# Performance work log

Measured on AMD Instinct MI355X. Metric: run time of the kernel, lower is better.

The kernel has to match this reference:

```python
import jax, jax.numpy as jnp
import numpy as np

V = 50000      # tokenizer vocab size
E = 128        # embedding_dim
H = 160        # encoder_hidden_dim (bidirectional -> 2H)
D = 196        # decoder_hidden_dim
A = 224        # attention_dim
BN = 56        # bottle_neck_dim
PAD, START, END, UNK = 0, 1, 2, 3
COV_FACTOR = 0.75


def _lstm_step(x, h, c, Wi, Wh, bi, bh):
    # torch gate order: i, f, g, o
    g = x @ Wi.T + h @ Wh.T + bi + bh
    i, f, gg, o = jnp.split(g, 4, axis=-1)
    c = jax.nn.sigmoid(f) * c + jax.nn.sigmoid(i) * jnp.tanh(gg)
    h = jax.nn.sigmoid(o) * jnp.tanh(c)
    return h, c


def _run_lstm(x_tbe, Wi, Wh, bi, bh):
    B = x_tbe.shape[1]
    Hh = Wh.shape[1]
    def step(carry, xt):
        h, c = carry
        h, c = _lstm_step(xt, h, c, Wi, Wh, bi, bh)
        return (h, c), h
    init = (jnp.zeros((B, Hh), x_tbe.dtype), jnp.zeros((B, Hh), x_tbe.dtype))
    (hT, cT), hs = jax.lax.scan(step, init, x_tbe)
    return hs, hT, cT


def setup_inputs() -> dict:
    key = jax.random.key(0)
    ks = iter(jax.random.split(key, 48))
    def rn(shape, s=0.05):
        return jax.random.normal(next(ks), shape, jnp.float32) * s
    B, Tin, Ttgt = 32, 256, 100
    inp = {
        'batch_input_ids': jax.random.randint(next(ks), (B, Tin), 0, V + 50, dtype=jnp.int32),
        'batch_target_ids': jax.random.randint(next(ks), (B, Ttgt), 0, V + 50, dtype=jnp.int32),
        'max_num_oovs': 50,
        'emb': rn((V, E), 0.1),
        # bidirectional encoder LSTM
        'Wi_f': rn((4 * H, E)), 'Wh_f': rn((4 * H, H)),
        'bi_f': jnp.zeros(4 * H), 'bh_f': jnp.zeros(4 * H),
        'Wi_b': rn((4 * H, E)), 'Wh_b': rn((4 * H, H)),
        'bi_b': jnp.zeros(4 * H), 'bh_b': jnp.zeros(4 * H),
        # enc->dec bridges
        'Weh': rn((D, 2 * H)), 'beh': jnp.zeros(D),
        'Wec': rn((D, 2 * H)), 'bec': jnp.zeros(D),
        # decoder LSTMCell
        'Wi_d': rn((4 * D, E)), 'Wh_d': rn((4 * D, D)),
        'bi_d': jnp.zeros(4 * D), 'bh_d': jnp.zeros(4 * D),
        # attention
        'Wea': rn((A, 2 * H)), 'bea': jnp.zeros(A),
        'Wda': rn((A, D)),
        'Wca': rn((A, 1)),
        'v_attn': rn((1, A)),
        # vocab projection (bottleneck)
        'W1': rn((BN, D + 2 * H)), 'b1': jnp.zeros(BN),
        'W2': rn((V - END, BN)), 'b2': jnp.zeros(V - END),
        # p_gen switch
        'Wcs': rn((1, 2 * H)), 'bcs': jnp.zeros(1),
        'Wds': rn((1, D)),
        'Wes': rn((1, E)),
    }
    return inp


def reference(batch_input_ids, batch_target_ids, max_num_oovs, emb,
              Wi_f, Wh_f, bi_f, bh_f, Wi_b, Wh_b, bi_b, bh_b,
              Weh, beh, Wec, bec, Wi_d, Wh_d, bi_d, bh_d,
              Wea, bea, Wda, Wca, v_attn, W1, b1, W2, b2,
              Wcs, bcs, Wds, Wes):
    B, Tin = batch_input_ids.shape
    # map OOV input ids to <unk> for embedding lookup
    in_mapped = jnp.where(batch_input_ids >= V, UNK, batch_input_ids)
    x_tbe = emb[in_mapped].transpose(1, 0, 2)          # [Tin,B,E]
    hs_f, hTf, cTf = _run_lstm(x_tbe, Wi_f, Wh_f, bi_f, bh_f)
    hs_b, hTb, cTb = _run_lstm(x_tbe[::-1], Wi_b, Wh_b, bi_b, bh_b)
    enc = jnp.concatenate([hs_f, hs_b[::-1]], -1).transpose(1, 0, 2)  # [B,Tin,2H]
    h = jnp.concatenate([hTf, hTb], -1) @ Weh.T + beh   # [B,D]
    c = jnp.concatenate([cTf, cTb], -1) @ Wec.T + bec   # [B,D]
    enc_attn = enc @ Wea.T + bea                        # [B,Tin,A] (loop-invariant)
    pad_mask = batch_input_ids == PAD
    wca = Wca[:, 0]                                     # [A]
    cov0 = jnp.zeros((B, Tin))
    cur0 = jnp.full((B,), START, jnp.int32)

    def step(carry, nt):
        h, c, cov, cur, nll, cl = carry
        e = emb[cur]                                     # [B,E]
        h, c = _lstm_step(e, h, c, Wi_d, Wh_d, bi_d, bh_d)
        s = jnp.tanh(enc_attn + (h @ Wda.T)[:, None, :] + cov[:, :, None] * wca)
        s = s @ v_attn[0]                                # [B,Tin]
        s = jnp.where(pad_mask, -jnp.inf, s)
        attn = jax.nn.softmax(s, axis=1)                 # [B,Tin]
        ctx = jnp.einsum('bt,bth->bh', attn, enc)        # [B,2H]
        hc = jnp.concatenate([h, ctx], -1)
        vocab = jax.nn.softmax(jnp.tanh(hc @ W1.T + b1) @ W2.T + b2, axis=1)  # [B,V-END]
        p_gen = jax.nn.sigmoid(ctx @ Wcs[0] + bcs[0] + h @ Wds[0] + e @ Wes[0])  # [B]
        # F.pad(vocab, (END, max_num_oovs)).gather(1, nt): left-pad END zeros,
        # right-pad OOV zeros -> gen prob is vocab[nt-END] if END<=nt<V else 0
        idx = jnp.clip(nt - END, 0, vocab.shape[1] - 1)
        gen_p = jnp.take_along_axis(vocab, idx[:, None], axis=1)[:, 0]
        gen_p = jnp.where((nt >= END) & (nt < V), gen_p, 0.0)
        copy_p = jnp.sum(attn * (batch_input_ids == nt[:, None]), axis=1)
        p = p_gen * gen_p + (1.0 - p_gen) * copy_p
        nll = nll - jnp.log(p + 1e-9)
        cl = cl + jnp.minimum(attn, cov).sum(axis=1)
        cov = cov + attn
        cur = jnp.where(nt >= V, UNK, nt)
        return (h, c, cov, cur, nll, cl), None

    (h, c, cov, cur, nll, cl), _ = jax.lax.scan(
        step, (h, c, cov0, cur0, jnp.zeros(B), jnp.zeros(B)), batch_target_ids.T)
    nll_loss = nll.sum()
    cov_loss = cl.sum()
    return nll_loss, cov_loss, nll_loss + COV_FACTOR * cov_loss
```

## Files before the change

### kernel.cpp

```cpp
#include <hip/hip_runtime.h>

#define MSCOPE __HIP_MEMORY_SCOPE_AGENT


constexpr size_t oXf   = 0;
constexpr size_t oXb   = oXf   + (size_t)8192*640;
constexpr size_t oXd   = oXb   + (size_t)8192*640;
constexpr size_t oHencB= oXd   + (size_t)3200*784;
constexpr size_t oEncA = oHencB+ (size_t)64*256*160;
constexpr size_t oEs   = oEncA + (size_t)8192*224;
constexpr size_t oCT   = oEs   + 3200;
constexpr size_t oH0   = oCT   + 10240;
constexpr size_t oC0   = oH0   + 6272;
constexpr size_t oHWdsAll = oC0 + 6272;
constexpr size_t oCtxWAll = oHWdsAll + 3200;
constexpr size_t oCopyAll = oCtxWAll + 3200;
constexpr size_t oZidxAll = oCopyAll + 3200;
constexpr size_t oClAll   = oZidxAll + 3200;
constexpr size_t oNllWg   = oClAll + 32;
constexpr size_t oW1cT    = oNllWg + 192;
constexpr size_t oFEnd    = oW1cT + 17920;
constexpr size_t oHdAll   = 0;
constexpr size_t oUAll    = oHdAll + (size_t)100*6272;
constexpr size_t oUPreAll = oUAll  + (size_t)100*1792;
constexpr size_t oHwdaAll = oUPreAll + (size_t)100*1792;
constexpr size_t oPartAll = oHwdaAll + (size_t)100*7168;
#define FENC(d,t,p)  ((((d)*256 + (t))*20 + (p))*16)
#define FLSTM(s,p)   (163840 + ((s)*25 + (p))*16)
#define FAUX(s,p)    (203840 + ((s)*8 + (p))*16)
#define FP2(s,m,p)   (216640 + (((s)*4 + (m))*32 + (p))*16)
#define CP3          421440
#define CFIN         421456
constexpr int fEnd = 421472;

__device__ __forceinline__ float fast_tanh(float x){
  float e = __expf(-2.f*fabsf(x));
  float r = (1.f - e) * __builtin_amdgcn_rcpf(1.f + e);
  return copysignf(r, x);
}
__device__ __forceinline__ float sigm(float x){
  return __builtin_amdgcn_rcpf(1.f + __expf(-x));
}
__device__ __forceinline__ float aload(const float* p){
  return __hip_atomic_load(const_cast<float*>(p), __ATOMIC_RELAXED, MSCOPE);
}
__device__ __forceinline__ float2 aload2(const float* p){
  unsigned long long u = __hip_atomic_load(
      reinterpret_cast<unsigned long long*>(const_cast<float*>(p)),
      __ATOMIC_RELAXED, MSCOPE);
  float2 r; __builtin_memcpy(&r, &u, 8); return r;
}
__device__ __forceinline__ void astore(float* p, float v){
  __hip_atomic_store(p, v, __ATOMIC_RELAXED, MSCOPE);
}
__device__ __forceinline__ void set_line(unsigned* line){
  __hip_atomic_store(line, 1u, __ATOMIC_RELAXED, MSCOPE);
}
template<int SLP>
__device__ __forceinline__ void wait_lines(unsigned* base, int n, int tid){
  if (tid < 64){
    for(;;){
      bool miss = (tid < n) &&
        (__hip_atomic_load(base + tid*16, __ATOMIC_RELAXED, MSCOPE) == 0u);
      if (__ballot(miss) == 0ULL) break;
      __builtin_amdgcn_s_sleep(SLP);
    }
  }
  __syncthreads();
}
__device__ __forceinline__ void add1(unsigned* word){
  (void)__hip_atomic_fetch_add(word, 1u, __ATOMIC_RELAXED, MSCOPE);
}
__device__ __forceinline__ float block_sum(float v, float* red){
  #pragma unroll
  for (int o=32;o;o>>=1) v += __shfl_down(v,o);
  if ((threadIdx.x&63)==0) red[threadIdx.x>>6] = v;
  __syncthreads();
  v = red[0]+red[1]+red[2]+red[3];
  __syncthreads();
  return v;
}

__global__ void prep_kernel(const int* __restrict__ in_ids, const int* __restrict__ tgt,
                            int* __restrict__ in_mapped, int* __restrict__ cur_ids,
                            unsigned* __restrict__ flags){
  const int g0 = blockIdx.x*256 + threadIdx.x, stride = gridDim.x*256;
  for (int i = g0; i < 8192; i += stride){
    int t = i >> 5, b = i & 31;
    int id = in_ids[b*256 + t];
    in_mapped[i] = (id >= 50000) ? 3 : id;
  }
  for (int i = g0; i < 3200; i += stride){
    int k = i >> 5, b = i & 31;
    int id = (k == 0) ? 1 : tgt[b*100 + (k-1)];
    cur_ids[i] = (id >= 50000) ? 3 : id;
  }
  for (int i = g0; i < fEnd; i += stride) flags[i] = 0u;
}

__global__ void w1c_transpose(const float* __restrict__ W1, float* __restrict__ W1cT){
  int i = blockIdx.x*256 + threadIdx.x;
  if (i < 17920){ int q = i / 56, g = i - q*56; W1cT[q*56+g] = W1[(size_t)g*516 + 196 + q]; }
}

struct RGArgs{ const int* gid; const float* emb; const float* W;
               const float* bias1; const float* bias2; float* out; int N; };
__global__ void __launch_bounds__(256) rowgemm(RGArgs a){
  __shared__ float rl[8*128];
  const int tid = threadIdx.x;
  const int N = a.N;
  const size_t r0 = (size_t)blockIdx.x*8;
  const size_t t = r0 >> 5; const int b0 = (int)(r0 & 31);
  for (int i = tid; i < 8*128; i += 256){
    int r = i >> 7, k = i & 127;
    rl[i] = a.emb[(size_t)a.gid[r0+r]*128 + k];
  }
  __syncthreads();
  for (int g = tid; g < N; g += 256){
    const float* wr = a.W + (size_t)g*128;
    float acc[8];
    #pragma unroll
    for (int r=0;r<8;r++) acc[r]=0.f;
    for (int k=0;k<128;k+=4){
      float4 wv = *(const float4*)(wr+k);
      #pragma unroll
      for (int r=0;r<8;r++){
        float4 xv = *(const float4*)(rl + r*128 + k);
        acc[r] += wv.x*xv.x + wv.y*xv.y + wv.z*xv.z + wv.w*xv.w;
      }
    }
    float bias = a.bias1[g] + a.bias2[g];
    float* op = a.out + ((size_t)t*N + g)*32 + b0;
    *(float4*)(op)   = make_float4(acc[0]+bias,acc[1]+bias,acc[2]+bias,acc[3]+bias);
    *(float4*)(op+4) = make_float4(acc[4]+bias,acc[5]+bias,acc[6]+bias,acc[7]+bias);
  }
}

__global__ void es_kernel(const int* __restrict__ gid, const float* __restrict__ emb,
                          const float* __restrict__ Wes, float* __restrict__ es){
  int r = blockIdx.x, l = threadIdx.x;
  const float* e = emb + (size_t)gid[r]*128;
  float acc = e[l]*Wes[l] + e[l+64]*Wes[l+64];
  #pragma unroll
  for (int o=32;o;o>>=1) acc += __shfl_down(acc,o);
  if (l==0) es[r] = acc;
}

struct EncArgs{ const float* Xf; const float* Xb; const float* Whf; const float* Whb;
                float* hencB; float* cT; unsigned* flg; };
__global__ void __launch_bounds__(256) enc_scan(EncArgs a){
  extern __shared__ float sm[];
  float* Wl = sm;
  float* hl = sm + 5120;
  const int wg = blockIdx.x;
  const int dir = wg/20, jwg = wg%20;
  const int tid = threadIdx.x;
  const int b = tid & 31, jl = tid >> 5;
  const int j = jwg*8 + jl;
  const float* Wh = dir ? a.Whb : a.Whf;
  const float* X  = dir ? a.Xb  : a.Xf;
  float* HB = a.hencB + (size_t)dir*32*256*160;
  unsigned* flg = a.flg;
  for (int i = tid; i < 32*160; i += 256){
    int row = i/160, k = i - row*160;
    int gate = row >> 3, jj = row & 7;
    Wl[i] = Wh[((size_t)(gate*160 + jwg*8 + jj))*160 + k];
  }
  for (int i = tid; i < 32*164; i += 256) hl[i] = 0.f;
  float c = 0.f;
  const float4* w0 = (const float4*)(Wl + (0*8+jl)*160);
  const float4* w1 = (const float4*)(Wl + (1*8+jl)*160);
  const float4* w2 = (const float4*)(Wl + (2*8+jl)*160);
  const float4* w3 = (const float4*)(Wl + (3*8+jl)*160);
  __syncthreads();
  for (int t = 0; t < 256; ++t){
    const int trow = dir ? 255 - t : t;
    const float* xr = X + ((size_t)trow*640 + j)*32 + b;
    float g0 = xr[0], g1 = xr[5120], g2 = xr[10240], g3 = xr[15360];
    if (t > 0){
      wait_lines<2>(flg + FENC(dir, t-1, 0), 20, tid);
      const int tprev = dir ? (256 - t) : (t-1);
      for (int i2 = tid; i2 < 2560; i2 += 256){
        int bb = i2/80, kk = (i2 - bb*80)*2;
        float2 v = aload2(HB + ((size_t)bb*256 + tprev)*160 + kk);
        *(float2*)(hl + bb*164 + kk) = v;
      }
    }
    __syncthreads();
    const float4* hr = (const float4*)(hl + b*164);
    #pragma unroll 4
    for (int q = 0; q < 40; ++q){
      float4 hv = hr[q];
      float4 a0 = w0[q], a1 = w1[q], a2 = w2[q], a3 = w3[q];
      g0 += hv.x*a0.x + hv.y*a0.y + hv.z*a0.z + hv.w*a0.w;
      g1 += hv.x*a1.x + hv.y*a1.y + hv.z*a1.z + hv.w*a1.w;
      g2 += hv.x*a2.x + hv.y*a2.y + hv.z*a2.z + hv.w*a2.w;
      g3 += hv.x*a3.x + hv.y*a3.y + hv.z*a3.z + hv.w*a3.w;
    }
    float ig = sigm(g0), fg = sigm(g1), gc = fast_tanh(g2), og = sigm(g3);
    c = fg*c + ig*gc;
    float h = og * fast_tanh(c);
    astore(&HB[((size_t)b*256 + trow)*160 + j], h);
    __syncthreads();
    if (tid == 0) set_line(flg + FENC(dir, t, jwg));
  }
  a.cT[dir*5120 + b*160 + j] = c;
}

__global__ void mid_kernel(const float* __restrict__ hencB, const float* __restrict__ cT,
                           const float* __restrict__ Weh, const float* __restrict__ beh,
                           const float* __restrict__ Wec, const float* __restrict__ bec,
                           float* __restrict__ h0, float* __restrict__ c0){
  __shared__ float hc[320], cc[320];
  int b = blockIdx.x, tid = threadIdx.x;
  if (tid < 160){
    hc[tid]     = hencB[((size_t)b*256 + 255)*160 + tid];
    hc[160+tid] = hencB[((size_t)(32+b)*256 + 0)*160 + tid];
    cc[tid]     = cT[b*160 + tid];
    cc[160+tid] = cT[5120 + b*160 + tid];
  }
  __syncthreads();
  for (int g = tid; g < 196; g += 256){
    const float* w1 = Weh + (size_t)g*320;
    const float* w2 = Wec + (size_t)g*320;
    float a1 = beh[g], a2 = bec[g];
    for (int k = 0; k < 320; ++k){ a1 += hc[k]*w1[k]; a2 += cc[k]*w2[k]; }
    h0[b*196 + g] = a1;
    c0[b*196 + g] = a2;
  }
}

__global__ void __launch_bounds__(256) encA_gemm(const float* __restrict__ hencB,
                 const float* __restrict__ Wea, const float* __restrict__ bea,
                 float* __restrict__ encA){
  __shared__ float rl[8*320];
  const int tid = threadIdx.x;
  const size_t r0 = (size_t)blockIdx.x*8;
  for (int i = tid; i < 8*320; i += 256){
    int r = i/320, k = i - r*320;
    size_t row = r0 + r; int b = (int)(row >> 8), t = (int)(row & 255);
    rl[i] = (k < 160) ? hencB[((size_t)b*256 + t)*160 + k]
                      : hencB[((size_t)(32+b)*256 + t)*160 + (k-160)];
  }
  __syncthreads();
  for (int g = tid; g < 224; g += 256){
    const float* wr = Wea + (size_t)g*320;
    float acc[8];
    #pragma unroll
    for (int r=0;r<8;r++) acc[r]=0.f;
    for (int k=0;k<320;k+=4){
      float4 wv = *(const float4*)(wr+k);
      #pragma unroll
      for (int r=0;r<8;r++){
        float4 xv = *(const float4*)(rl + r*320 + k);
        acc[r] += wv.x*xv.x + wv.y*xv.y + wv.z*xv.z + wv.w*xv.w;
      }
    }
    float bias = bea[g];
    #pragma unroll
    for (int r=0;r<8;r++) encA[(r0+r)*224 + g] = acc[r] + bias;
  }
}

struct DecArgs{
  const float* Xd; const float* hencB; const float* encA;
  const float* h0; const float* c0;
  const float* Whd; const float* Wda; const float* Wca; const float* vat;
  const float* W1; const float* b1; const float* W1cT; const float* W2; const float* b2;
  const float* Wcs; const float* bcs; const float* Wds; const float* es;
  const int* in_ids; const int* tgt;
  float* hdAll; float* uAll; float* uPreAll; float* hwdaAll;
  float* hWdsAll; float* ctxWAll; float* copyAll;
  float* zidxAll; float* partAll; float* clAll; float* nllWg; float* out;
  unsigned* flg;
};

__device__ __forceinline__ void load_scr(const float* hp, float* scr, int tid){
  for (int i2 = tid; i2 < 3136; i2 += 256){
    float2 hv = aload2(hp + i2*2);
    int e = i2*2; int b2 = e & 31; int j2 = e >> 5;
    scr[b2*204 + j2]     = hv.x;
    scr[(b2+1)*204 + j2] = hv.y;
  }
}

__global__ void __launch_bounds__(256) dec_scan(DecArgs A){
  extern __shared__ float sm[];
  const int wg = blockIdx.x, tid = threadIdx.x;
  const int bp = tid & 31, jl = tid >> 5;
  unsigned* flg = A.flg;

  if (wg < 25){
    const int wl = wg;
    const int j = wl*8 + jl;
    float* Wl  = sm;
    float* scr = sm + 6272;
    for (int i = tid; i < 32*196; i += 256){
      int row = i/196, k = i - row*196;
      int gate = row >> 3, jj = row & 7;
      int jg = wl*8 + jj;
      Wl[i] = (jg < 196) ? A.Whd[((size_t)(gate*196 + jg))*196 + k] : 0.f;
    }
    float c = (j < 196) ? A.c0[bp*196 + j] : 0.f;
    for (int i = tid; i < 6272; i += 256){
      int bb = i/196, k = i - bb*196;
      scr[bb*204 + k] = A.h0[i];
    }
    const float4* w0 = (const float4*)(Wl + (0*8+jl)*196);
    const float4* w1 = (const float4*)(Wl + (1*8+jl)*196);
    const float4* w2 = (const float4*)(Wl + (2*8+jl)*196);
    const float4* w3 = (const float4*)(Wl + (3*8+jl)*196);
    __syncthreads();
    for (int s = 0; s < 100; ++s){
      float x0=0.f,x1=0.f,x2=0.f,x3=0.f;
      if (j < 196){
        const float* xr = A.Xd + ((size_t)s*784 + j)*32 + bp;
        x0 = xr[0]; x1 = xr[6272]; x2 = xr[12544]; x3 = xr[18816];
      }
      if (s > 0){
        wait_lines<2>(flg + FLSTM(s-1, 0), 25, tid);
        load_scr(A.hdAll + (size_t)(s-1)*6272, scr, tid);
      }
      __syncthreads();
      if (j < 196){
        float g0=x0,g1=x1,g2=x2,g3=x3;
        const float4* hr = (const float4*)(scr + bp*204);
        #pragma unroll 7
        for (int q = 0; q < 49; ++q){
          float4 hv = hr[q];
          float4 a0 = w0[q], a1 = w1[q], a2 = w2[q], a3 = w3[q];
          g0 += hv.x*a0.x + hv.y*a0.y + hv.z*a0.z + hv.w*a0.w;
          g1 += hv.x*a1.x + hv.y*a1.y + hv.z*a1.z + hv.w*a1.w;
          g2 += hv.x*a2.x + hv.y*a2.y + hv.z*a2.z + hv.w*a2.w;
          g3 += hv.x*a3.x + hv.y*a3.y + hv.z*a3.z + hv.w*a3.w;
        }
        float ig = sigm(g0), fg = sigm(g1), gc = fast_tanh(g2), og = sigm(g3);
        c = fg*c + ig*gc;
        float h = og * fast_tanh(c);
        astore(&A.hdAll[(size_t)s*6272 + j*32 + bp], h);
      }
      __syncthreads();
      if (tid == 0) set_line(flg + FLSTM(s, wl));
    }
    return;
  }

  if (wg < 33){
    const int a_ = wg - 25;
    float* wdaL = sm;
    float* w1hL = sm + 5488;
    float* WdsL = sm + 6860;
    float* scr  = sm + 7056;
    for (int i = tid; i < 28*196; i += 256){
      int al = i/196, k = i - al*196;
      wdaL[i] = A.Wda[(size_t)(a_*28 + al)*196 + k];
    }
    for (int i = tid; i < 7*196; i += 256){
      int gl = i/196, k = i - gl*196;
      w1hL[i] = A.W1[(size_t)(a_*7 + gl)*516 + k];
    }
    if (a_ == 7) for (int i = tid; i < 196; i += 256) WdsL[i] = A.Wds[i];
    __syncthreads();
    for (int s = 0; s < 100; ++s){
      wait_lines<2>(flg + FLSTM(s, 0), 25, tid);
      load_scr(A.hdAll + (size_t)s*6272, scr, tid);
      __syncthreads();
      for (int i = tid; i < 896; i += 256){
        int b2 = i & 31, al = i >> 5;
        const float4* h4 = (const float4*)(scr + b2*204);
        const float4* w4 = (const float4*)(wdaL + al*196);
        float acc = 0.f;
        #pragma unroll 7
        for (int q = 0; q < 49; ++q){
          float4 a4 = h4[q], b4 = w4[q];
          acc += a4.x*b4.x + a4.y*b4.y + a4.z*b4.z + a4.w*b4.w;
        }
        astore(&A.hwdaAll[(size_t)s*7168 + b2*224 + a_*28 + al], acc);
      }
      if (tid < 224){
        int b2 = tid & 31, gl = tid >> 5;
        int g = a_*7 + gl;
        const float4* h4 = (const float4*)(scr + b2*204);
        const float4* w4 = (const float4*)(w1hL + gl*196);
        float acc = A.b1[g];
        #pragma unroll 7
        for (int q = 0; q < 49; ++q){
          float4 a4 = h4[q], b4 = w4[q];
          acc += a4.x*b4.x + a4.y*b4.y + a4.z*b4.z + a4.w*b4.w;
        }
        astore(&A.uPreAll[(size_t)s*1792 + b2*56 + g], acc);
      }
      if (a_ == 7 && tid < 32){
        const float* hb = scr + tid*204;
        float acc = 0.f;
        #pragma unroll 4
        for (int q = 0; q < 196; ++q) acc += hb[q]*WdsL[q];
        astore(&A.hWdsAll[s*32 + tid], acc);
      }
      __syncthreads();
      if (tid == 0) set_line(flg + FAUX(s, a_));
    }
    return;
  }

  if (wg < 65){
    const int b = wg - 33;
    float* hwdaL = sm;
    float* attnL = sm + 224;
    float* pctx  = sm + 480;
    float* ctxL  = sm + 1440;
    float* red   = sm + 1760;
    float* pu    = sm + 1764;
    float* wcaL  = sm + 1988;
    float* vL    = sm + 2212;
    float* WcsL  = sm + 2436;
    if (tid < 224){ wcaL[tid] = A.Wca[tid]; vL[tid] = A.vat[tid]; }
    for (int i = tid; i < 320; i += 256) WcsL[i] = A.Wcs[i];
    const int inid = A.in_ids[b*256 + tid];
    const float4* erow = (const float4*)(A.encA + (size_t)(b*256 + tid)*224);
    float cov = 0.f, clr = 0.f;
    __syncthreads();
    for (int s = 0; s < 100; ++s){
      wait_lines<2>(flg + FAUX(s, 0), 8, tid);
      if (tid < 224) hwdaL[tid] = aload(&A.hwdaAll[(size_t)s*7168 + b*224 + tid]);
      __syncthreads();
      float exv = 0.f;
      if (inid != 0){
        float acc = 0.f;
        #pragma unroll 8
        for (int q = 0; q < 56; ++q){
          float4 ev = erow[q]; int a0 = 4*q;
          acc += fast_tanh(ev.x + hwdaL[a0]   + cov*wcaL[a0]  )*vL[a0];
          acc += fast_tanh(ev.y + hwdaL[a0+1] + cov*wcaL[a0+1])*vL[a0+1];
          acc += fast_tanh(ev.z + hwdaL[a0+2] + cov*wcaL[a0+2])*vL[a0+2];
          acc += fast_tanh(ev.w + hwdaL[a0+3] + cov*wcaL[a0+3])*vL[a0+3];
        }
        exv = __expf(acc);
      }
      float S = block_sum(exv, red);
      float attn = exv * __builtin_amdgcn_rcpf(S);
      attnL[tid] = attn;
      const int ntb = A.tgt[b*100 + s];
      float cpS = block_sum((inid == ntb) ? attn : 0.f, red);
      float mnS = block_sum(fminf(attn, cov), red);
      if (tid == 0){
        astore(&A.copyAll[s*32 + b], cpS);
        clr += mnS;
        if (s == 99) astore(&A.clAll[b], clr);
      }
      cov += attn;
      if (tid < 240){
        int seg = tid/80, h4i = tid - seg*80;
        int t0 = seg*86, t1 = (t0+86 < 256) ? t0+86 : 256;
        const float* base = (h4i < 40)
          ? (A.hencB + ((size_t)b*256)*160 + (size_t)h4i*4)
          : (A.hencB + ((size_t)(32+b)*256)*160 + (size_t)(h4i-40)*4);
        float4 accv = {0.f,0.f,0.f,0.f};
        #pragma unroll 4
        for (int t2 = t0; t2 < t1; ++t2){
          float av = attnL[t2];
          float4 ev = *(const float4*)(base + (size_t)t2*160);
          accv.x += av*ev.x; accv.y += av*ev.y; accv.z += av*ev.z; accv.w += av*ev.w;
        }
        *(float4*)(pctx + (seg*80+h4i)*4) = accv;
      }
      __syncthreads();
      if (tid < 80){
        float4 p0 = *(float4*)(pctx + tid*4);
        float4 p1 = *(float4*)(pctx + (80+tid)*4);
        float4 p2v = *(float4*)(pctx + (160+tid)*4);
        float4 cvv;
        cvv.x = p0.x+p1.x+p2v.x; cvv.y = p0.y+p1.y+p2v.y;
        cvv.z = p0.z+p1.z+p2v.z; cvv.w = p0.w+p1.w+p2v.w;
        *(float4*)(ctxL + tid*4) = cvv;
      }
      __syncthreads();
      if (tid < 224){
        int g = tid % 56, seg = tid / 56;
        float acc = 0.f;
        const float* wp = A.W1cT + (size_t)seg*80*56 + g;
        #pragma unroll 4
        for (int q = 0; q < 80; ++q) acc += ctxL[seg*80 + q] * wp[q*56];
        pu[seg*56 + g] = acc;
      } else {
        int l = tid - 224; float acc = 0.f;
        for (int q = l; q < 320; q += 32) acc += ctxL[q]*WcsL[q];
        #pragma unroll
        for (int o=16;o;o>>=1) acc += __shfl_down(acc,o,32);
        if (l==0) astore(&A.ctxWAll[s*32 + b], acc);
      }
      __syncthreads();
      if (tid < 56){
        float upre = aload(&A.uPreAll[(size_t)s*1792 + b*56 + tid]);
        float uu = fast_tanh(upre + pu[tid] + pu[56+tid] + pu[112+tid] + pu[168+tid]);
        astore(&A.uAll[(size_t)s*1792 + b*56 + tid], uu);
      }
      __syncthreads();
      if (tid == 0){
        set_line(flg + FP2(s,0,b));
        set_line(flg + FP2(s,1,b));
        set_line(flg + FP2(s,2,b));
        set_line(flg + FP2(s,3,b));
      }
    }
    return;
  }

  {
    const int wgv = wg - 65;
    const int vs = (int)(((long long)wgv*49998)/191);
    const int ve = (int)(((long long)(wgv+1)*49998)/191);
    const int r0v = vs + tid;
    const int r1v = vs + 256 + tid;
    const bool v1 = r1v < ve;
    float4 w2r0[14], w2r1[14];
    {
      const float4* wr = (const float4*)(A.W2 + (size_t)r0v*56);
      #pragma unroll
      for (int q=0;q<14;++q) w2r0[q] = wr[q];
      const float4* wr1 = (const float4*)(A.W2 + (size_t)(v1 ? r1v : vs)*56);
      #pragma unroll
      for (int q=0;q<14;++q) w2r1[q] = wr1[q];
    }
    const float b2v0 = A.b2[r0v];
    const float b2v1 = v1 ? A.b2[r1v] : 0.f;
    float* ulL  = sm;
    float* redW = sm + 1792;
    int*   idxL = (int*)(sm + 1920);
    float* red  = sm + 1952;
    const int lane = tid & 63, wv2 = tid >> 6;
    for (int s = 0; s < 100; ++s){
      int nt3 = (tid < 32) ? A.tgt[tid*100 + s] : 0;
      wait_lines<8>(flg + FP2(s, wgv & 3, 0), 32, tid);
      for (int i2 = tid; i2 < 896; i2 += 256){
        float2 u2 = aload2(&A.uAll[(size_t)s*1792 + i2*2]);
        *(float2*)(ulL + i2*2) = u2;
      }
      if (tid < 32){
        int ix = nt3 - 2; ix = ix<0?0:(ix>49997?49997:ix);
        idxL[tid] = ix;
      }
      __syncthreads();
      #pragma unroll 4
      for (int bb=0; bb<32; ++bb){
        const float4* uv = (const float4*)(ulL + bb*56);
        float z = b2v0;
        #pragma unroll
        for (int q=0;q<14;++q){
          float4 u4 = uv[q];
          z += w2r0[q].x*u4.x + w2r0[q].y*u4.y + w2r0[q].z*u4.z + w2r0[q].w*u4.w;
        }
        if (r0v == idxL[bb]) astore(&A.zidxAll[s*32+bb], z);
        float sv2 = __expf(z);
        if (v1){
          float z1 = b2v1;
          #pragma unroll
          for (int q=0;q<14;++q){
            float4 u4 = uv[q];
            z1 += w2r1[q].x*u4.x + w2r1[q].y*u4.y + w2r1[q].z*u4.z + w2r1[q].w*u4.w;
          }
          if (r1v == idxL[bb]) astore(&A.zidxAll[s*32+bb], z1);
          sv2 += __expf(z1);
        }
        #pragma unroll
        for (int o=32;o;o>>=1) sv2 += __shfl_down(sv2,o);
        if (lane == 0) redW[wv2*32+bb] = sv2;
      }
      __syncthreads();
      if (tid < 32){
        float tot = redW[tid]+redW[32+tid]+redW[64+tid]+redW[96+tid];
        astore(&A.partAll[(size_t)(s*32+tid)*191 + wgv], tot);
      }
      __syncthreads();
    }
    __syncthreads();
    if (tid == 0) add1(flg + CP3);
    if (tid == 0){
      while (__hip_atomic_load(flg + CP3, __ATOMIC_RELAXED, MSCOPE) != 191u)
        __builtin_amdgcn_s_sleep(32);
    }
    __syncthreads();
    float nll1 = 0.f;
    for (int p = wgv; p < 3200; p += 191){
      float pv = (tid < 191) ? aload(&A.partAll[(size_t)p*191 + tid]) : 0.f;
      float se = block_sum(pv, red);
      if (tid == 0){
        int s = p >> 5, b = p & 31;
        int nt2 = A.tgt[b*100 + s];
        float xg = aload(&A.ctxWAll[p]) + A.bcs[0] + aload(&A.hWdsAll[p]) + A.es[p];
        float pg = 1.f/(1.f + __expf(-xg));
        float genp = (nt2 >= 2 && nt2 < 50000) ? (__expf(aload(&A.zidxAll[p])) / se) : 0.f;
        float pr = pg*genp + (1.f-pg)*aload(&A.copyAll[p]);
        nll1 += -logf(pr + 1e-9f);
      }
    }
    if (tid == 0) astore(&A.nllWg[wgv], nll1);
    __syncthreads();
    if (tid == 0) add1(flg + CFIN);
    if (wg == 65){
      if (tid == 0){
        while (__hip_atomic_load(flg + CFIN, __ATOMIC_RELAXED, MSCOPE) != 191u)
          __builtin_amdgcn_s_sleep(32);
      }
      __syncthreads();
      float nv = (tid < 191) ? aload(&A.nllWg[tid]) : 0.f;
      float nll = block_sum(nv, red);
      float cv = (tid < 32) ? aload(&A.clAll[tid]) : 0.f;
      float cl = block_sum(cv, red);
      if (tid == 0){ A.out[0]=nll; A.out[1]=cl; A.out[2]=nll + 0.75f*cl; }
    }
  }
}

extern "C" void kernel_launch(void* const* d_in, const int* in_sizes, int n_in,
                              void* d_out, int out_size, void* d_ws, size_t ws_size,
                              hipStream_t stream){
  const int*   in_ids = (const int*)  d_in[0];
  const int*   tgt    = (const int*)  d_in[1];
  const float* emb    = (const float*)d_in[3];
  const float* Wi_f   = (const float*)d_in[4];
  const float* Wh_f   = (const float*)d_in[5];
  const float* bi_f   = (const float*)d_in[6];
  const float* bh_f   = (const float*)d_in[7];
  const float* Wi_b   = (const float*)d_in[8];
  const float* Wh_b   = (const float*)d_in[9];
  const float* bi_b   = (const float*)d_in[10];
  const float* bh_b   = (const float*)d_in[11];
  const float* Weh    = (const float*)d_in[12];
  const float* beh    = (const float*)d_in[13];
  const float* Wec    = (const float*)d_in[14];
  const float* bec    = (const float*)d_in[15];
  const float* Wi_d   = (const float*)d_in[16];
  const float* Wh_d   = (const float*)d_in[17];
  const float* bi_d   = (const float*)d_in[18];
  const float* bh_d   = (const float*)d_in[19];
  const float* Wea    = (const float*)d_in[20];
  const float* bea    = (const float*)d_in[21];
  const float* Wda    = (const float*)d_in[22];
  const float* Wca    = (const float*)d_in[23];
  const float* vat    = (const float*)d_in[24];
  const float* W1     = (const float*)d_in[25];
  const float* b1     = (const float*)d_in[26];
  const float* W2     = (const float*)d_in[27];
  const float* b2     = (const float*)d_in[28];
  const float* Wcs    = (const float*)d_in[29];
  const float* bcs    = (const float*)d_in[30];
  const float* Wds    = (const float*)d_in[31];
  const float* Wes    = (const float*)d_in[32];

  float* ws = (float*)d_ws;
  int* iBase = (int*)(ws + oFEnd);
  int* in_mapped = iBase;
  int* cur_ids   = iBase + 8192;
  unsigned* flags = (unsigned*)(iBase + 11392);

  prep_kernel<<<512, 256, 0, stream>>>(in_ids, tgt, in_mapped, cur_ids, flags);
  w1c_transpose<<<70, 256, 0, stream>>>(W1, ws + oW1cT);

  { RGArgs a{in_mapped, emb, Wi_f, bi_f, bh_f, ws + oXf, 640};
    rowgemm<<<1024, 256, 0, stream>>>(a); }
  { RGArgs a{in_mapped, emb, Wi_b, bi_b, bh_b, ws + oXb, 640};
    rowgemm<<<1024, 256, 0, stream>>>(a); }
  { RGArgs a{cur_ids, emb, Wi_d, bi_d, bh_d, ws + oXd, 784};
    rowgemm<<<400, 256, 0, stream>>>(a); }

  es_kernel<<<3200, 64, 0, stream>>>(cur_ids, emb, Wes, ws + oEs);

  { EncArgs ea{ws + oXf, ws + oXb, Wh_f, Wh_b, ws + oHencB, ws + oCT, flags};
    void* ka[] = {&ea};
    hipLaunchCooperativeKernel((void*)enc_scan, dim3(40), dim3(256), ka,
                               (unsigned)((5120 + 32*164)*4), stream); }

  mid_kernel<<<32, 256, 0, stream>>>(ws + oHencB, ws + oCT, Weh, beh, Wec, bec,
                                     ws + oH0, ws + oC0);

  encA_gemm<<<1024, 256, 0, stream>>>(ws + oHencB, Wea, bea, ws + oEncA);

  { DecArgs da{ws + oXd, ws + oHencB, ws + oEncA,
               ws + oH0, ws + oC0,
               Wh_d, Wda, Wca, vat,
               W1, b1, ws + oW1cT, W2, b2, Wcs, bcs, Wds, ws + oEs,
               in_ids, tgt,
               ws + oHdAll, ws + oUAll, ws + oUPreAll, ws + oHwdaAll,
               ws + oHWdsAll, ws + oCtxWAll, ws + oCopyAll,
               ws + oZidxAll, ws + oPartAll, ws + oClAll, ws + oNllWg, (float*)d_out,
               flags};
    void* ka[] = {&da};
    hipLaunchCooperativeKernel((void*)dec_scan, dim3(256), dim3(256), ka,
                               (unsigned)(13584*4), stream); }
}
```

Baseline: 4.925 ms.

## Split fused decoder scan into separate chain, attention, vocab and finalize kernels

The single cooperative 256-workgroup decoder kernel pipelined four roles across steps: LSTM chain, attention, vocab projection and final reduction, synchronised by per-step flags. It is replaced by five ordinary launches in sequence: an LSTM plus projection chain kernel, a per-batch attention kernel, a vocab softmax-partials kernel on 224 blocks, and two reduction kernels. This works because, with teacher forcing, the LSTM never depends on the attention output. The change removes cross-role flag polling and atomic loads and stores, and gives the vocab stage a wider, simpler grid. The cost is that cross-stage overlap is lost, so the attention and vocab work now runs after the chain finishes instead of alongside it.

```diff
diff --git a/kernel.cpp b/kernel.cpp
--- a/kernel.cpp
+++ b/kernel.cpp
@@ -17,8 +17,8 @@
 constexpr size_t oCopyAll = oCtxWAll + 3200;
 constexpr size_t oZidxAll = oCopyAll + 3200;
 constexpr size_t oClAll   = oZidxAll + 3200;
-constexpr size_t oNllWg   = oClAll + 32;
-constexpr size_t oW1cT    = oNllWg + 192;
+constexpr size_t oNllB    = oClAll + 32;
+constexpr size_t oW1cT    = oNllB + 32;
 constexpr size_t oFEnd    = oW1cT + 17920;
 constexpr size_t oHdAll   = 0;
 constexpr size_t oUAll    = oHdAll + (size_t)100*6272;
@@ -27,11 +27,8 @@
 constexpr size_t oPartAll = oHwdaAll + (size_t)100*7168;
 #define FENC(d,t,p)  ((((d)*256 + (t))*20 + (p))*16)
 #define FLSTM(s,p)   (163840 + ((s)*25 + (p))*16)
-#define FAUX(s,p)    (203840 + ((s)*8 + (p))*16)
-#define FP2(s,m,p)   (216640 + (((s)*4 + (m))*32 + (p))*16)
-#define CP3          421440
-#define CFIN         421456
-constexpr int fEnd = 421472;
+constexpr int fEnd = 203840;
+constexpr unsigned ENC_FULL  = 0xFFFFFu;
 
 __device__ __forceinline__ float fast_tanh(float x){
   float e = __expf(-2.f*fabsf(x));
@@ -53,6 +50,9 @@
 __device__ __forceinline__ void astore(float* p, float v){
   __hip_atomic_store(p, v, __ATOMIC_RELAXED, MSCOPE);
 }
+__device__ __forceinline__ unsigned uload(unsigned* p){
+  return __hip_atomic_load(p, __ATOMIC_RELAXED, MSCOPE);
+}
 __device__ __forceinline__ void set_line(unsigned* line){
   __hip_atomic_store(line, 1u, __ATOMIC_RELAXED, MSCOPE);
 }
@@ -60,16 +60,12 @@
 __device__ __forceinline__ void wait_lines(unsigned* base, int n, int tid){
   if (tid < 64){
     for(;;){
-      bool miss = (tid < n) &&
-        (__hip_atomic_load(base + tid*16, __ATOMIC_RELAXED, MSCOPE) == 0u);
+      bool miss = (tid < n) && (uload(base + tid*16) == 0u);
       if (__ballot(miss) == 0ULL) break;
       __builtin_amdgcn_s_sleep(SLP);
     }
   }
   __syncthreads();
-}
-__device__ __forceinline__ void add1(unsigned* word){
-  (void)__hip_atomic_fetch_add(word, 1u, __ATOMIC_RELAXED, MSCOPE);
 }
 __device__ __forceinline__ float block_sum(float v, float* red){
   #pragma unroll
@@ -262,16 +258,11 @@
   }
 }
 
-struct DecArgs{
-  const float* Xd; const float* hencB; const float* encA;
-  const float* h0; const float* c0;
-  const float* Whd; const float* Wda; const float* Wca; const float* vat;
-  const float* W1; const float* b1; const float* W1cT; const float* W2; const float* b2;
-  const float* Wcs; const float* bcs; const float* Wds; const float* es;
-  const int* in_ids; const int* tgt;
-  float* hdAll; float* uAll; float* uPreAll; float* hwdaAll;
-  float* hWdsAll; float* ctxWAll; float* copyAll;
-  float* zidxAll; float* partAll; float* clAll; float* nllWg; float* out;
+struct ChainArgs{
+  const float* Xd; const float* h0; const float* c0;
+  const float* Whd; const float* Wda; const float* W1; const float* Wds;
+  const float* b1;
+  float* hdAll; float* hwdaAll; float* uPreAll; float* hWdsAll;
   unsigned* flg;
 };
 
@@ -284,7 +275,7 @@
   }
 }
 
-__global__ void __launch_bounds__(256) dec_scan(DecArgs A){
+__global__ void __launch_bounds__(256) dec_chain(ChainArgs A){
   extern __shared__ float sm[];
   const int wg = blockIdx.x, tid = threadIdx.x;
   const int bp = tid & 31, jl = tid >> 5;
@@ -345,7 +336,7 @@
     return;
   }
 
-  if (wg < 33){
+  {
     const int a_ = wg - 25;
     float* wdaL = sm;
     float* w1hL = sm + 5488;
@@ -375,7 +366,7 @@
           float4 a4 = h4[q], b4 = w4[q];
           acc += a4.x*b4.x + a4.y*b4.y + a4.z*b4.z + a4.w*b4.w;
         }
-        astore(&A.hwdaAll[(size_t)s*7168 + b2*224 + a_*28 + al], acc);
+        A.hwdaAll[(size_t)s*7168 + b2*224 + a_*28 + al] = acc;
       }
       if (tid < 224){
         int b2 = tid & 31, gl = tid >> 5;
@@ -388,228 +379,214 @@
           float4 a4 = h4[q], b4 = w4[q];
           acc += a4.x*b4.x + a4.y*b4.y + a4.z*b4.z + a4.w*b4.w;
         }
-        astore(&A.uPreAll[(size_t)s*1792 + b2*56 + g], acc);
+        A.uPreAll[(size_t)s*1792 + b2*56 + g] = acc;
       }
       if (a_ == 7 && tid < 32){
         const float* hb = scr + tid*204;
         float acc = 0.f;
         #pragma unroll 4
         for (int q = 0; q < 196; ++q) acc += hb[q]*WdsL[q];
-        astore(&A.hWdsAll[s*32 + tid], acc);
+        A.hWdsAll[s*32 + tid] = acc;
       }
       __syncthreads();
-      if (tid == 0) set_line(flg + FAUX(s, a_));
-    }
-    return;
-  }
-
-  if (wg < 65){
-    const int b = wg - 33;
-    float* hwdaL = sm;
-    float* attnL = sm + 224;
-    float* pctx  = sm + 480;
-    float* ctxL  = sm + 1440;
-    float* red   = sm + 1760;
-    float* pu    = sm + 1764;
-    float* wcaL  = sm + 1988;
-    float* vL    = sm + 2212;
-    float* WcsL  = sm + 2436;
-    if (tid < 224){ wcaL[tid] = A.Wca[tid]; vL[tid] = A.vat[tid]; }
-    for (int i = tid; i < 320; i += 256) WcsL[i] = A.Wcs[i];
-    const int inid = A.in_ids[b*256 + tid];
-    const float4* erow = (const float4*)(A.encA + (size_t)(b*256 + tid)*224);
-    float cov = 0.f, clr = 0.f;
-    __syncthreads();
-    for (int s = 0; s < 100; ++s){
-      wait_lines<2>(flg + FAUX(s, 0), 8, tid);
-      if (tid < 224) hwdaL[tid] = aload(&A.hwdaAll[(size_t)s*7168 + b*224 + tid]);
-      __syncthreads();
-      float exv = 0.f;
-      if (inid != 0){
-        float acc = 0.f;
-        #pragma unroll 8
-        for (int q = 0; q < 56; ++q){
-          float4 ev = erow[q]; int a0 = 4*q;
-          acc += fast_tanh(ev.x + hwdaL[a0]   + cov*wcaL[a0]  )*vL[a0];
-          acc += fast_tanh(ev.y + hwdaL[a0+1] + cov*wcaL[a0+1])*vL[a0+1];
-          acc += fast_tanh(ev.z + hwdaL[a0+2] + cov*wcaL[a0+2])*vL[a0+2];
-          acc += fast_tanh(ev.w + hwdaL[a0+3] + cov*wcaL[a0+3])*vL[a0+3];
-        }
-        exv = __expf(acc);
-      }
-      float S = block_sum(exv, red);
-      float attn = exv * __builtin_amdgcn_rcpf(S);
-      attnL[tid] = attn;
-      const int ntb = A.tgt[b*100 + s];
-      float cpS = block_sum((inid == ntb) ? attn : 0.f, red);
-      float mnS = block_sum(fminf(attn, cov), red);
-      if (tid == 0){
-        astore(&A.copyAll[s*32 + b], cpS);
-        clr += mnS;
-        if (s == 99) astore(&A.clAll[b], clr);
-      }
-      cov += attn;
-      if (tid < 240){
-        int seg = tid/80, h4i = tid - seg*80;
-        int t0 = seg*86, t1 = (t0+86 < 256) ? t0+86 : 256;
-        const float* base = (h4i < 40)
-          ? (A.hencB + ((size_t)b*256)*160 + (size_t)h4i*4)
-          : (A.hencB + ((size_t)(32+b)*256)*160 + (size_t)(h4i-40)*4);
-        float4 accv = {0.f,0.f,0.f,0.f};
-        #pragma unroll 4
-        for (int t2 = t0; t2 < t1; ++t2){
-          float av = attnL[t2];
-          float4 ev = *(const float4*)(base + (size_t)t2*160);
-          accv.x += av*ev.x; accv.y += av*ev.y; accv.z += av*ev.z; accv.w += av*ev.w;
-        }
-        *(float4*)(pctx + (seg*80+h4i)*4) = accv;
-      }
-      __syncthreads();
-      if (tid < 80){
-        float4 p0 = *(float4*)(pctx + tid*4);
-        float4 p1 = *(float4*)(pctx + (80+tid)*4);
-        float4 p2v = *(float4*)(pctx + (160+tid)*4);
-        float4 cvv;
-        cvv.x = p0.x+p1.x+p2v.x; cvv.y = p0.y+p1.y+p2v.y;
-        cvv.z = p0.z+p1.z+p2v.z; cvv.w = p0.w+p1.w+p2v.w;
-        *(float4*)(ctxL + tid*4) = cvv;
-      }
-      __syncthreads();
-      if (tid < 224){
-        int g = tid % 56, seg = tid / 56;
-        float acc = 0.f;
-        const float* wp = A.W1cT + (size_t)seg*80*56 + g;
-        #pragma unroll 4
-        for (int q = 0; q < 80; ++q) acc += ctxL[seg*80 + q] * wp[q*56];
-        pu[seg*56 + g] = acc;
-      } else {
-        int l = tid - 224; float acc = 0.f;
-        for (int q = l; q < 320; q += 32) acc += ctxL[q]*WcsL[q];
-        #pragma unroll
-        for (int o=16;o;o>>=1) acc += __shfl_down(acc,o,32);
-        if (l==0) astore(&A.ctxWAll[s*32 + b], acc);
-      }
-      __syncthreads();
-      if (tid < 56){
-        float upre = aload(&A.uPreAll[(size_t)s*1792 + b*56 + tid]);
-        float uu = fast_tanh(upre + pu[tid] + pu[56+tid] + pu[112+tid] + pu[168+tid]);
-        astore(&A.uAll[(size_t)s*1792 + b*56 + tid], uu);
-      }
-      __syncthreads();
-      if (tid == 0){
-        set_line(flg + FP2(s,0,b));
-        set_line(flg + FP2(s,1,b));
-        set_line(flg + FP2(s,2,b));
-        set_line(flg + FP2(s,3,b));
-      }
-    }
-    return;
-  }
-
+    }
+  }
+}
+
+struct AttArgs{
+  const float* hencB; const float* encA;
+  const float* Wca; const float* vat; const float* W1cT; const float* Wcs;
+  const float* hwdaAll; const float* uPreAll;
+  const int* in_ids; const int* tgt;
+  float* uAll; float* ctxWAll; float* copyAll; float* clAll;
+};
+
+__global__ void __launch_bounds__(256) dec_att(AttArgs A){
+  __shared__ float sm[2812];
+  const int b = blockIdx.x, tid = threadIdx.x;
+  float* hwdaL = sm;
+  float* attnL = sm + 224;
+  float* pctx  = sm + 480;
+  float* ctxL  = sm + 1440;
+  float* red   = sm + 1760;
+  float* pu    = sm + 1764;
+  float* wcaL  = sm + 1988;
+  float* vL    = sm + 2212;
+  float* WcsL  = sm + 2436;
+  if (tid < 224){ wcaL[tid] = A.Wca[tid]; vL[tid] = A.vat[tid]; }
+  for (int i = tid; i < 320; i += 256) WcsL[i] = A.Wcs[i];
+  const int inid = A.in_ids[b*256 + tid];
+  const float4* erow = (const float4*)(A.encA + (size_t)(b*256 + tid)*224);
+  float cov = 0.f, clr = 0.f;
+  __syncthreads();
+  for (int s = 0; s < 100; ++s){
+    if (tid < 224) hwdaL[tid] = A.hwdaAll[(size_t)s*7168 + b*224 + tid];
+    __syncthreads();
+    float exv = 0.f;
+    if (inid != 0){
+      float acc = 0.f;
+      #pragma unroll 8
+      for (int q = 0; q < 56; ++q){
+        float4 ev = erow[q]; int a0 = 4*q;
+        acc += fast_tanh(ev.x + hwdaL[a0]   + cov*wcaL[a0]  )*vL[a0];
+        acc += fast_tanh(ev.y + hwdaL[a0+1] + cov*wcaL[a0+1])*vL[a0+1];
+        acc += fast_tanh(ev.z + hwdaL[a0+2] + cov*wcaL[a0+2])*vL[a0+2];
+        acc += fast_tanh(ev.w + hwdaL[a0+3] + cov*wcaL[a0+3])*vL[a0+3];
+      }
+      exv = __expf(acc);
+    }
+    float S = block_sum(exv, red);
+    float attn = exv * __builtin_amdgcn_rcpf(S);
+    attnL[tid] = attn;
+    const int ntb = A.tgt[b*100 + s];
+    float cpS = block_sum((inid == ntb) ? attn : 0.f, red);
+    float mnS = block_sum(fminf(attn, cov), red);
+    if (tid == 0){
+      A.copyAll[s*32 + b] = cpS;
+      clr += mnS;
+      if (s == 99) A.clAll[b] = clr;
+    }
+    cov += attn;
+    if (tid < 240){
+      int seg = tid/80, h4i = tid - seg*80;
+      int t0 = seg*86, t1 = (t0+86 < 256) ? t0+86 : 256;
+      const float* base = (h4i < 40)
+        ? (A.hencB + ((size_t)b*256)*160 + (size_t)h4i*4)
+        : (A.hencB + ((size_t)(32+b)*256)*160 + (size_t)(h4i-40)*4);
+      float4 accv = {0.f,0.f,0.f,0.f};
+      #pragma unroll 4
+      for (int t2 = t0; t2 < t1; ++t2){
+        float av = attnL[t2];
+        float4 ev = *(const float4*)(base + (size_t)t2*160);
+        accv.x += av*ev.x; accv.y += av*ev.y; accv.z += av*ev.z; accv.w += av*ev.w;
+      }
+      *(float4*)(pctx + (seg*80+h4i)*4) = accv;
+    }
+    __syncthreads();
+    if (tid < 80){
+      float4 p0 = *(float4*)(pctx + tid*4);
+      float4 p1 = *(float4*)(pctx + (80+tid)*4);
+      float4 p2v = *(float4*)(pctx + (160+tid)*4);
+      float4 cvv;
+      cvv.x = p0.x+p1.x+p2v.x; cvv.y = p0.y+p1.y+p2v.y;
+      cvv.z = p0.z+p1.z+p2v.z; cvv.w = p0.w+p1.w+p2v.w;
+      *(float4*)(ctxL + tid*4) = cvv;
+    }
+    __syncthreads();
+    if (tid < 224){
+      int g = tid % 56, seg = tid / 56;
+      float acc = 0.f;
+      const float* wp = A.W1cT + (size_t)seg*80*56 + g;
+      #pragma unroll 4
+      for (int q = 0; q < 80; ++q) acc += ctxL[seg*80 + q] * wp[q*56];
+      pu[seg*56 + g] = acc;
+    } else {
+      int l = tid - 224; float acc = 0.f;
+      for (int q = l; q < 320; q += 32) acc += ctxL[q]*WcsL[q];
+      #pragma unroll
+      for (int o=16;o;o>>=1) acc += __shfl_down(acc,o,32);
+      if (l==0) A.ctxWAll[s*32 + b] = acc;
+    }
+    __syncthreads();
+    if (tid < 56){
+      float upre = A.uPreAll[(size_t)s*1792 + b*56 + tid];
+      A.uAll[(size_t)s*1792 + b*56 + tid] =
+        fast_tanh(upre + pu[tid] + pu[56+tid] + pu[112+tid] + pu[168+tid]);
+    }
+    __syncthreads();
+  }
+}
+
+struct VocArgs{
+  const float* W2; const float* b2; const float* uAll; const int* tgt;
+  float* zidxAll; float* partAll;
+};
+
+__global__ void __launch_bounds__(256) dec_voc(VocArgs A){
+  __shared__ float ulL[1792];
+  __shared__ float redW[128];
+  __shared__ int idxL[32];
+  const int wgv = blockIdx.x, tid = threadIdx.x;
+  const int vs = (int)(((long long)wgv*49998)/224);
+  const int ve = (int)(((long long)(wgv+1)*49998)/224);
+  const int v = vs + tid;
+  const bool valid = v < ve;
+  const int vc = valid ? v : 0;
+  float4 w2r[14];
   {
-    const int wgv = wg - 65;
-    const int vs = (int)(((long long)wgv*49998)/191);
-    const int ve = (int)(((long long)(wgv+1)*49998)/191);
-    const int r0v = vs + tid;
-    const int r1v = vs + 256 + tid;
-    const bool v1 = r1v < ve;
-    float4 w2r0[14], w2r1[14];
-    {
-      const float4* wr = (const float4*)(A.W2 + (size_t)r0v*56);
+    const float4* wr = (const float4*)(A.W2 + (size_t)vc*56);
+    #pragma unroll
+    for (int q=0;q<14;++q) w2r[q] = wr[q];
+  }
+  const float b2v = A.b2[vc];
+  const int lane = tid & 63, wv2 = tid >> 6;
+  for (int s = 0; s < 100; ++s){
+    for (int i = tid; i < 448; i += 256)
+      *(float4*)(ulL + i*4) = *(const float4*)(&A.uAll[(size_t)s*1792 + i*4]);
+    if (tid < 32){
+      int nt3 = A.tgt[tid*100 + s];
+      int ix = nt3 - 2; ix = ix<0?0:(ix>49997?49997:ix);
+      idxL[tid] = ix;
+    }
+    __syncthreads();
+    #pragma unroll 4
+    for (int bb=0; bb<32; ++bb){
+      const float4* uv = (const float4*)(ulL + bb*56);
+      float z = b2v;
       #pragma unroll
-      for (int q=0;q<14;++q) w2r0[q] = wr[q];
-      const float4* wr1 = (const float4*)(A.W2 + (size_t)(v1 ? r1v : vs)*56);
+      for (int q=0;q<14;++q){
+        float4 u4 = uv[q];
+        z += w2r[q].x*u4.x + w2r[q].y*u4.y + w2r[q].z*u4.z + w2r[q].w*u4.w;
+      }
+      if (valid && v == idxL[bb]) A.zidxAll[s*32+bb] = z;
+      float sv2 = valid ? __expf(z) : 0.f;
       #pragma unroll
-      for (int q=0;q<14;++q) w2r1[q] = wr1[q];
-    }
-    const float b2v0 = A.b2[r0v];
-    const float b2v1 = v1 ? A.b2[r1v] : 0.f;
-    float* ulL  = sm;
-    float* redW = sm + 1792;
-    int*   idxL = (int*)(sm + 1920);
-    float* red  = sm + 1952;
-    const int lane = tid & 63, wv2 = tid >> 6;
-    for (int s = 0; s < 100; ++s){
-      int nt3 = (tid < 32) ? A.tgt[tid*100 + s] : 0;
-      wait_lines<8>(flg + FP2(s, wgv & 3, 0), 32, tid);
-      for (int i2 = tid; i2 < 896; i2 += 256){
-        float2 u2 = aload2(&A.uAll[(size_t)s*1792 + i2*2]);
-        *(float2*)(ulL + i2*2) = u2;
-      }
-      if (tid < 32){
-        int ix = nt3 - 2; ix = ix<0?0:(ix>49997?49997:ix);
-        idxL[tid] = ix;
-      }
-      __syncthreads();
-      #pragma unroll 4
-      for (int bb=0; bb<32; ++bb){
-        const float4* uv = (const float4*)(ulL + bb*56);
-        float z = b2v0;
-        #pragma unroll
-        for (int q=0;q<14;++q){
-          float4 u4 = uv[q];
-          z += w2r0[q].x*u4.x + w2r0[q].y*u4.y + w2r0[q].z*u4.z + w2r0[q].w*u4.w;
-        }
-        if (r0v == idxL[bb]) astore(&A.zidxAll[s*32+bb], z);
-        float sv2 = __expf(z);
-        if (v1){
-          float z1 = b2v1;
-          #pragma unroll
-          for (int q=0;q<14;++q){
-            float4 u4 = uv[q];
-            z1 += w2r1[q].x*u4.x + w2r1[q].y*u4.y + w2r1[q].z*u4.z + w2r1[q].w*u4.w;
-          }
-          if (r1v == idxL[bb]) astore(&A.zidxAll[s*32+bb], z1);
-          sv2 += __expf(z1);
-        }
-        #pragma unroll
-        for (int o=32;o;o>>=1) sv2 += __shfl_down(sv2,o);
-        if (lane == 0) redW[wv2*32+bb] = sv2;
-      }
-      __syncthreads();
-      if (tid < 32){
-        float tot = redW[tid]+redW[32+tid]+redW[64+tid]+redW[96+tid];
-        astore(&A.partAll[(size_t)(s*32+tid)*191 + wgv], tot);
-      }
-      __syncthreads();
-    }
-    __syncthreads();
-    if (tid == 0) add1(flg + CP3);
+      for (int o=32;o;o>>=1) sv2 += __shfl_down(sv2,o);
+      if (lane == 0) redW[wv2*32+bb] = sv2;
+    }
+    __syncthreads();
+    if (tid < 32)
+      A.partAll[(size_t)(s*32+tid)*224 + wgv] =
+        redW[tid]+redW[32+tid]+redW[64+tid]+redW[96+tid];
+    __syncthreads();
+  }
+}
+
+struct Fin1Args{
+  const float* partAll; const int* tgt;
+  const float* ctxWAll; const float* hWdsAll; const float* es;
+  const float* zidxAll; const float* copyAll; const float* bcs;
+  float* nllB;
+};
+__global__ void __launch_bounds__(256) dec_fin1(Fin1Args A){
+  __shared__ float red[4];
+  const int b = blockIdx.x, tid = threadIdx.x;
+  float nll = 0.f;
+  const float bcs0 = A.bcs[0];
+  for (int s = 0; s < 100; ++s){
+    int p = s*32 + b;
+    float pv = (tid < 224) ? A.partAll[(size_t)p*224 + tid] : 0.f;
+    float se = block_sum(pv, red);
     if (tid == 0){
-      while (__hip_atomic_load(flg + CP3, __ATOMIC_RELAXED, MSCOPE) != 191u)
-        __builtin_amdgcn_s_sleep(32);
-    }
-    __syncthreads();
-    float nll1 = 0.f;
-    for (int p = wgv; p < 3200; p += 191){
-      float pv = (tid < 191) ? aload(&A.partAll[(size_t)p*191 + tid]) : 0.f;
-      float se = block_sum(pv, red);
-      if (tid == 0){
-        int s = p >> 5, b = p & 31;
-        int nt2 = A.tgt[b*100 + s];
-        float xg = aload(&A.ctxWAll[p]) + A.bcs[0] + aload(&A.hWdsAll[p]) + A.es[p];
-        float pg = 1.f/(1.f + __expf(-xg));
-        float genp = (nt2 >= 2 && nt2 < 50000) ? (__expf(aload(&A.zidxAll[p])) / se) : 0.f;
-        float pr = pg*genp + (1.f-pg)*aload(&A.copyAll[p]);
-        nll1 += -logf(pr + 1e-9f);
-      }
-    }
-    if (tid == 0) astore(&A.nllWg[wgv], nll1);
-    __syncthreads();
-    if (tid == 0) add1(flg + CFIN);
-    if (wg == 65){
-      if (tid == 0){
-        while (__hip_atomic_load(flg + CFIN, __ATOMIC_RELAXED, MSCOPE) != 191u)
-          __builtin_amdgcn_s_sleep(32);
-      }
-      __syncthreads();
-      float nv = (tid < 191) ? aload(&A.nllWg[tid]) : 0.f;
-      float nll = block_sum(nv, red);
-      float cv = (tid < 32) ? aload(&A.clAll[tid]) : 0.f;
-      float cl = block_sum(cv, red);
-      if (tid == 0){ A.out[0]=nll; A.out[1]=cl; A.out[2]=nll + 0.75f*cl; }
-    }
-  }
+      int nt2 = A.tgt[b*100 + s];
+      float xg = A.ctxWAll[p] + bcs0 + A.hWdsAll[p] + A.es[p];
+      float pg = 1.f/(1.f + __expf(-xg));
+      float genp = (nt2 >= 2 && nt2 < 50000) ? (__expf(A.zidxAll[p]) / se) : 0.f;
+      float pr = pg*genp + (1.f-pg)*A.copyAll[p];
+      nll += -logf(pr + 1e-9f);
+    }
+  }
+  if (tid == 0) A.nllB[b] = nll;
+}
+
+__global__ void dec_fin2(const float* __restrict__ nllB, const float* __restrict__ clAll,
+                         float* __restrict__ out){
+  int tid = threadIdx.x;
+  float n = (tid < 32) ? nllB[tid] : 0.f;
+  float cv = (tid < 32) ? clAll[tid] : 0.f;
+  #pragma unroll
+  for (int o=32;o;o>>=1){ n += __shfl_down(n,o); cv += __shfl_down(cv,o); }
+  if (tid == 0){ out[0]=n; out[1]=cv; out[2]=n + 0.75f*cv; }
 }
 
 extern "C" void kernel_launch(void* const* d_in, const int* in_sizes, int n_in,
@@ -676,16 +653,26 @@
 
   encA_gemm<<<1024, 256, 0, stream>>>(ws + oHencB, Wea, bea, ws + oEncA);
 
-  { DecArgs da{ws + oXd, ws + oHencB, ws + oEncA,
-               ws + oH0, ws + oC0,
-               Wh_d, Wda, Wca, vat,
-               W1, b1, ws + oW1cT, W2, b2, Wcs, bcs, Wds, ws + oEs,
+  { ChainArgs ca{ws + oXd, ws + oH0, ws + oC0,
+                 Wh_d, Wda, W1, Wds, b1,
+                 ws + oHdAll, ws + oHwdaAll, ws + oUPreAll, ws + oHWdsAll,
+                 flags};
+    dec_chain<<<dim3(33), dim3(256), 13584*4, stream>>>(ca); }
+
+  { AttArgs aa{ws + oHencB, ws + oEncA,
+               Wca, vat, ws + oW1cT, Wcs,
+               ws + oHwdaAll, ws + oUPreAll,
                in_ids, tgt,
-               ws + oHdAll, ws + oUAll, ws + oUPreAll, ws + oHwdaAll,
-               ws + oHWdsAll, ws + oCtxWAll, ws + oCopyAll,
-               ws + oZidxAll, ws + oPartAll, ws + oClAll, ws + oNllWg, (float*)d_out,
-               flags};
-    void* ka[] = {&da};
-    hipLaunchCooperativeKernel((void*)dec_scan, dim3(256), dim3(256), ka,
-                               (unsigned)(13584*4), stream); }
-}
+               ws + oUAll, ws + oCtxWAll, ws + oCopyAll, ws + oClAll};
+    dec_att<<<dim3(32), dim3(256), 0, stream>>>(aa); }
+
+  { VocArgs va{W2, b2, ws + oUAll, tgt, ws + oZidxAll, ws + oPartAll};
+    dec_voc<<<dim3(224), dim3(256), 0, stream>>>(va); }
+
+  { Fin1Args fa{ws + oPartAll, tgt, ws + oCtxWAll, ws + oHWdsAll, ws + oEs,
+                ws + oZidxAll, ws + oCopyAll, bcs, ws + oNllB};
+    dec_fin1<<<dim3(32), dim3(256), 0, stream>>>(fa); }
+
+  dec_fin2<<<dim3(1), dim3(64), 0, stream>>>(ws + oNllB, ws + oClAll,
+                                             (float*)d_out);
+}
```

After: 6.487 ms. +31.7%, slower.
